# Kernel optimization log

Hardware: AMD Instinct MI355X
Metric: run time of the kernel (lower is better)

## Reference

```python
import jax, jax.numpy as jnp
import numpy as np

B, LQ, LK, D, H, DK, DV = 4, 2048, 2048, 1024, 16, 64, 64
TEMP = float(np.sqrt(DK))
LN_EPS = 1e-5


def setup_inputs() -> dict:
    key = jax.random.key(0)
    ks = jax.random.split(key, 12)
    std_qk = float(np.sqrt(2.0 / (D + DK)))
    std_v = float(np.sqrt(2.0 / (D + DV)))
    std_fc = float(np.sqrt(2.0 / (H * DV + D)))  # xavier normal
    return {
        "q": jax.random.normal(ks[0], (B, LQ, D), jnp.float32),
        "k": jax.random.normal(ks[1], (B, LK, D), jnp.float32),
        "v": jax.random.normal(ks[2], (B, LK, D), jnp.float32),
        "key_padding_mask": jax.random.randint(ks[3], (B, LK), 0, 2) > 0,
        "Wq": jax.random.normal(ks[4], (D, H * DK), jnp.float32) * std_qk,
        "bq": jnp.zeros((H * DK,), jnp.float32),
        "Wk": jax.random.normal(ks[5], (D, H * DK), jnp.float32) * std_qk,
        "bk": jnp.zeros((H * DK,), jnp.float32),
        "Wv": jax.random.normal(ks[6], (D, H * DV), jnp.float32) * std_v,
        "bv": jnp.zeros((H * DV,), jnp.float32),
        "Wo": jax.random.normal(ks[7], (H * DV, D), jnp.float32) * std_fc,
        "bo": jnp.zeros((D,), jnp.float32),
        "ln_g": jnp.ones((D,), jnp.float32),
        "ln_b": jnp.zeros((D,), jnp.float32),
    }


def reference(q, k, v, key_padding_mask, Wq, bq, Wk, bk, Wv, bv, Wo, bo, ln_g, ln_b):
    residual = q
    # projections -> [B, H, L, dh]
    qh = (q @ Wq + bq).reshape(B, LQ, H, DK).transpose(0, 2, 1, 3)
    kh = (k @ Wk + bk).reshape(B, LK, H, DK).transpose(0, 2, 1, 3)
    vh = (v @ Wv + bv).reshape(B, LK, H, DV).transpose(0, 2, 1, 3)
    # scaled dot-product attention, mask padded keys with -inf pre-softmax
    logits = jnp.einsum("bhqd,bhkd->bhqk", qh, kh) / TEMP
    logits = jnp.where(key_padding_mask[:, None, None, :], -jnp.inf, logits)
    attn = jax.nn.softmax(logits, axis=-1)  # masked entries -> 0
    out = jnp.einsum("bhqk,bhkd->bhqd", attn, vh)
    # concat heads (head-major per original permute) -> [B, LQ, H*DV]
    out = out.transpose(0, 2, 1, 3).reshape(B, LQ, H * DV)
    out = out @ Wo + bo
    out = out + residual  # skip connection (d_out == d_model)
    # LayerNorm over last dim
    mu = out.mean(-1, keepdims=True)
    var = ((out - mu) ** 2).mean(-1, keepdims=True)
    out = (out - mu) * jax.lax.rsqrt(var + LN_EPS) * ln_g + ln_b
    attn_avg = attn.mean(axis=1)  # average over heads -> [B, LQ, LK]
    return out, attn_avg
```

## Files before the change

kernel.cpp:

```cpp
#include <hip/hip_runtime.h>
#include <hip/hip_bf16.h>
#include <math.h>

#define B_    4
#define LQ_   2048
#define LK_   2048
#define D_    1024
#define H_    16
#define LN_EPS_ 1e-5f
#define NEGINF (-__builtin_inff())
#define QSCALE 0.18033688011112042f

typedef __attribute__((ext_vector_type(8))) short bf16x8;
typedef __attribute__((ext_vector_type(4))) short bf16x4;
typedef __attribute__((ext_vector_type(4))) float f32x4;

#define MFMA(a, b, c) __builtin_amdgcn_mfma_f32_16x16x32_bf16(a, b, c, 0, 0, 0)

#if __has_builtin(__builtin_amdgcn_exp2f)
#define EXP2(x) __builtin_amdgcn_exp2f(x)
#else
#define EXP2(x) __expf((x) * 0.6931471805599453f)
#endif

__device__ __forceinline__ short f2bf(float f) {
    union { __hip_bfloat16 h; short s; } u;
    u.h = __float2bfloat16(f);
    return u.s;
}

__device__ __forceinline__ void gld16(const short* g, short* l) {
    __builtin_amdgcn_global_load_lds(
        (const __attribute__((address_space(1))) void*)g,
        (__attribute__((address_space(3))) void*)l, 16, 0, 0);
}

__global__ __launch_bounds__(256) void zfill_kernel(float* __restrict__ p)
{
    const size_t i = ((size_t)blockIdx.x * 256 + threadIdx.x) * 4;
    *reinterpret_cast<f32x4*>(p + i) = (f32x4){0.f, 0.f, 0.f, 0.f};
}

__global__ __launch_bounds__(256) void scan_kernel(
    const int* __restrict__ mask, int* __restrict__ idx, int* __restrict__ pos,
    int* __restrict__ cnt, float* __restrict__ maskc)
{
    const int b = blockIdx.x;
    const int t = threadIdx.x;
    const int lane = t & 63, wid = t >> 6;
    __shared__ int wsum[4];
    const int base = b * 2048 + t * 8;

    int fl[8]; int loc = 0;
    #pragma unroll
    for (int j = 0; j < 8; ++j) { fl[j] = (mask[base + j] == 0) ? 1 : 0; loc += fl[j]; }

    int inc = loc;
    #pragma unroll
    for (int d = 1; d < 64; d <<= 1) {
        const int n = __shfl_up(inc, d);
        if (lane >= d) inc += n;
    }
    if (lane == 63) wsum[wid] = inc;
    __syncthreads();
    int wbase = 0;
    for (int i = 0; i < wid; ++i) wbase += wsum[i];
    const int total = wsum[0] + wsum[1] + wsum[2] + wsum[3];

    int e = wbase + inc - loc;
    #pragma unroll
    for (int j = 0; j < 8; ++j) {
        const int p = t * 8 + j;
        if (fl[j]) { idx[b * 2048 + e] = p; pos[base + j] = e; ++e; }
        else        pos[base + j] = -1;
        maskc[base + j] = (p < total) ? 0.f : NEGINF;
        if (p >= total) idx[base + j] = 0;
    }
    if (t == 0) cnt[b] = total;
}

__global__ __launch_bounds__(256) void cast_x_kernel(
    const float* __restrict__ q, const float* __restrict__ k, const float* __restrict__ v,
    short* __restrict__ Xq, short* __restrict__ Xk, short* __restrict__ Xv)
{
    const int which = blockIdx.y;
    const float* src = which == 0 ? q : (which == 1 ? k : v);
    short* dst       = which == 0 ? Xq : (which == 1 ? Xk : Xv);
    const int t = threadIdx.x;
    const size_t i = ((size_t)blockIdx.x * 256 + t) * 8;
    const float4 a = *reinterpret_cast<const float4*>(src + i);
    const float4 c = *reinterpret_cast<const float4*>(src + i + 4);
    bf16x8 o;
    o[0] = f2bf(a.x); o[1] = f2bf(a.y); o[2] = f2bf(a.z); o[3] = f2bf(a.w);
    o[4] = f2bf(c.x); o[5] = f2bf(c.y); o[6] = f2bf(c.z); o[7] = f2bf(c.w);
    *reinterpret_cast<bf16x8*>(dst + i) = o;
}

__global__ __launch_bounds__(256) void cast_wt_kernel(
    const float* __restrict__ Wq, const float* __restrict__ Wk,
    const float* __restrict__ Wv, const float* __restrict__ Wo,
    short* __restrict__ Wtq, short* __restrict__ Wtk,
    short* __restrict__ Wtv, short* __restrict__ Wto)
{
    const int which = blockIdx.z;
    const float* W = which == 0 ? Wq : (which == 1 ? Wk : (which == 2 ? Wv : Wo));
    short* Wt      = which == 0 ? Wtq : (which == 1 ? Wtk : (which == 2 ? Wtv : Wto));

    __shared__ float T[64][65];
    const int t = threadIdx.x;
    const int k0 = blockIdx.x * 64, n0 = blockIdx.y * 64;
    {
        const int row = t >> 2, cq = (t & 3) * 16;
        #pragma unroll
        for (int i = 0; i < 4; ++i) {
            const float4 v4 = *reinterpret_cast<const float4*>(&W[(size_t)(k0 + row) * 1024 + n0 + cq + i * 4]);
            T[row][cq + i * 4 + 0] = v4.x; T[row][cq + i * 4 + 1] = v4.y;
            T[row][cq + i * 4 + 2] = v4.z; T[row][cq + i * 4 + 3] = v4.w;
        }
    }
    __syncthreads();
    const int nl = t >> 2, kq = (t & 3) * 16;
    bf16x8 o0, o1;
    #pragma unroll
    for (int j = 0; j < 8; ++j) {
        o0[j] = f2bf(T[kq + j][nl]);
        o1[j] = f2bf(T[kq + 8 + j][nl]);
    }
    *reinterpret_cast<bf16x8*>(&Wt[(size_t)(n0 + nl) * 1024 + k0 + kq]) = o0;
    *reinterpret_cast<bf16x8*>(&Wt[(size_t)(n0 + nl) * 1024 + k0 + kq + 8]) = o1;
}

__global__ __launch_bounds__(256) void proj_kernel(
    const short* __restrict__ Xq, const short* __restrict__ Xk, const short* __restrict__ Xv,
    const short* __restrict__ Wtq, const short* __restrict__ Wtk, const short* __restrict__ Wtv,
    const float* __restrict__ bq, const float* __restrict__ bk, const float* __restrict__ bv,
    const int* __restrict__ pos,
    short* __restrict__ qh, short* __restrict__ kh, short* __restrict__ vTc)
{
    const int which = blockIdx.z;
    const short* A  = which == 0 ? Xq : (which == 1 ? Xk : Xv);
    const short* Bt = which == 0 ? Wtq : (which == 1 ? Wtk : Wtv);
    const float* bias = which == 0 ? bq : (which == 1 ? bk : bv);

    __shared__ short Al[4096];
    __shared__ short Bl[4096];

    const int t = threadIdx.x;
    const int lane = t & 63, w = t >> 6;
    const int wm = w >> 1, wn = w & 1;
    const int g = lane >> 4, r16 = lane & 15;
    const int m0 = blockIdx.y * 128, n0 = blockIdx.x * 128;

    f32x4 acc[4][4] = {};

    for (int k0 = 0; k0 < 1024; k0 += 32) {
        __syncthreads();
        #pragma unroll
        for (int i = 0; i < 2; ++i) {
            const int row = i * 64 + (t >> 2);
            const int cl = (t & 3) ^ ((row >> 1) & 3);
            gld16(A  + (size_t)(m0 + row) * 1024 + k0 + cl * 8, Al + i * 2048 + t * 8);
            gld16(Bt + (size_t)(n0 + row) * 1024 + k0 + cl * 8, Bl + i * 2048 + t * 8);
        }
        __syncthreads();

        bf16x8 af[4], bf[4];
        #pragma unroll
        for (int mf = 0; mf < 4; ++mf) {
            const int row = wm * 64 + mf * 16 + r16;
            af[mf] = *reinterpret_cast<const bf16x8*>(
                (const char*)Al + row * 64 + (((g ^ ((row >> 1) & 3))) << 4));
        }
        #pragma unroll
        for (int nf = 0; nf < 4; ++nf) {
            const int row = wn * 64 + nf * 16 + r16;
            bf[nf] = *reinterpret_cast<const bf16x8*>(
                (const char*)Bl + row * 64 + (((g ^ ((row >> 1) & 3))) << 4));
        }
        #pragma unroll
        for (int mf = 0; mf < 4; ++mf)
            #pragma unroll
            for (int nf = 0; nf < 4; ++nf)
                acc[mf][nf] = MFMA(af[mf], bf[nf], acc[mf][nf]);
    }

    if (which < 2) {
        #pragma unroll
        for (int nf = 0; nf < 4; ++nf) {
            const int n = n0 + wn * 64 + nf * 16 + r16;
            const int h = n >> 6, dh = n & 63;
            const float bn = bias[n];
            #pragma unroll
            for (int mf = 0; mf < 4; ++mf) {
                #pragma unroll
                for (int r = 0; r < 4; ++r) {
                    const int m = m0 + wm * 64 + mf * 16 + 4 * g + r;
                    const int bb = m >> 11, l = m & 2047;
                    float vf = acc[mf][nf][r] + bn;
                    if (which == 0) vf *= QSCALE;
                    ((which == 0) ? qh : kh)[(((size_t)(bb * H_ + h)) * LQ_ + l) * 64 + dh] = f2bf(vf);
                }
            }
        }
    } else {
        int posr[4][4], bbr[4][4];
        #pragma unroll
        for (int mf = 0; mf < 4; ++mf)
            #pragma unroll
            for (int r = 0; r < 4; ++r) {
                const int m = m0 + wm * 64 + mf * 16 + 4 * g + r;
                const int bb = m >> 11, l = m & 2047;
                bbr[mf][r] = bb;
                posr[mf][r] = pos[bb * 2048 + l];
            }
        #pragma unroll
        for (int nf = 0; nf < 4; ++nf) {
            const int n = n0 + wn * 64 + nf * 16 + r16;
            const int h = n >> 6, dh = n & 63;
            const float bn = bias[n];
            #pragma unroll
            for (int mf = 0; mf < 4; ++mf) {
                #pragma unroll
                for (int r = 0; r < 4; ++r) {
                    const int pc = posr[mf][r];
                    if (pc >= 0)
                        vTc[(((size_t)(bbr[mf][r] * H_ + h)) * 64 + dh) * (size_t)LK_ + pc] =
                            f2bf(acc[mf][nf][r] + bn);
                }
            }
        }
    }
}

__global__ __launch_bounds__(256) void flash_kernel(
    const short* __restrict__ qh, const short* __restrict__ kh, const short* __restrict__ vTc,
    const int* __restrict__ idx, const int* __restrict__ cnt, const float* __restrict__ maskc,
    short* __restrict__ ctx, float* __restrict__ mOut, float* __restrict__ sOut)
{
    const int q0 = blockIdx.x * 64;
    const int h  = blockIdx.y;
    const int b  = blockIdx.z;

    __shared__ short Kl[2][4096];
    __shared__ short Vl[2][4096];

    const int t = threadIdx.x;
    const int lane = t & 63, w = t >> 6;
    const int g = lane >> 4, q16 = lane & 15;

    const short* kbase = kh + (size_t)(b * H_ + h) * LK_ * 64;
    const short* vbase = vTc + (size_t)(b * H_ + h) * 64 * (size_t)LK_;
    const int*   idxb  = idx + b * 2048;
    const int nt = (cnt[b] + 63) >> 6;

    bf16x8 qf0, qf1;
    {
        const short* qrow = qh + ((size_t)(b * H_ + h) * LQ_ + q0 + w * 16 + q16) * 64;
        qf0 = *reinterpret_cast<const bf16x8*>(qrow + 8 * g);
        qf1 = *reinterpret_cast<const bf16x8*>(qrow + 32 + 8 * g);
    }

    f32x4 mlast[4] = {};
    if (nt > 0) {
        #pragma unroll
        for (int kb = 0; kb < 4; ++kb)
            mlast[kb] = *reinterpret_cast<const f32x4*>(
                maskc + b * 2048 + (nt - 1) * 64 + kb * 16 + 4 * g);
    }

    const int srw = t >> 3, scl = t & 7;

    f32x4 ot[4] = {};
    float m_run = NEGINF, l_run = 0.f;

    if (nt > 0) {
        #pragma unroll
        for (int i = 0; i < 2; ++i) {
            const int row = i * 32 + srw;
            const int cl = scl ^ (row & 7);
            const int orig = idxb[row];
            gld16(kbase + (size_t)orig * 64 + cl * 8, Kl[0] + i * 2048 + t * 8);
            gld16(vbase + (size_t)row * LK_ + cl * 8, Vl[0] + i * 2048 + t * 8);
        }
    }
    __syncthreads();

    int cur = 0;
    for (int kt = 0; kt < nt; ++kt) {
        if (kt + 1 < nt) {
            const int kn = (kt + 1) * 64;
            #pragma unroll
            for (int i = 0; i < 2; ++i) {
                const int row = i * 32 + srw;
                const int cl = scl ^ (row & 7);
                const int orig = idxb[kn + row];
                gld16(kbase + (size_t)orig * 64 + cl * 8, Kl[cur ^ 1] + i * 2048 + t * 8);
                gld16(vbase + (size_t)row * LK_ + kn + cl * 8, Vl[cur ^ 1] + i * 2048 + t * 8);
            }
        }
        const bool lastt = (kt == nt - 1);

        float lg[4][4];
        const short* klp = Kl[cur];
        __builtin_amdgcn_s_setprio(1);
        #pragma unroll
        for (int kb = 0; kb < 4; ++kb) {
            const int krow = kb * 16 + q16;
            const char* rowp = (const char*)klp + krow * 128;
            const int sw = (krow & 7) << 4;
            const bf16x8 kf0 = *reinterpret_cast<const bf16x8*>(rowp + ((g << 4) ^ sw));
            const bf16x8 kf1 = *reinterpret_cast<const bf16x8*>(rowp + (((4 + g) << 4) ^ sw));
            f32x4 s = lastt ? mlast[kb] : (f32x4){0.f, 0.f, 0.f, 0.f};
            s = MFMA(kf0, qf0, s);
            s = MFMA(kf1, qf1, s);
            #pragma unroll
            for (int r = 0; r < 4; ++r) lg[kb][r] = s[r];
        }
        __builtin_amdgcn_s_setprio(0);

        float tm = NEGINF;
        #pragma unroll
        for (int kb = 0; kb < 4; ++kb)
            #pragma unroll
            for (int r = 0; r < 4; ++r) tm = fmaxf(tm, lg[kb][r]);
        tm = fmaxf(tm, __shfl_xor(tm, 16));
        tm = fmaxf(tm, __shfl_xor(tm, 32));

        const bool skip = __all(tm <= m_run + 8.0f);
        if (!skip) {
            const float m_new = fmaxf(m_run, tm);
            const float alpha = (m_run == NEGINF) ? 0.f : EXP2(m_run - m_new);
            #pragma unroll
            for (int fc = 0; fc < 4; ++fc)
                #pragma unroll
                for (int r = 0; r < 4; ++r) ot[fc][r] *= alpha;
            l_run *= alpha;
            m_run = m_new;
        }
        const float m_use = (m_run == NEGINF) ? 0.f : m_run;

        float p[4][4];
        float ls = 0.f;
        #pragma unroll
        for (int kb = 0; kb < 4; ++kb)
            #pragma unroll
            for (int r = 0; r < 4; ++r) { p[kb][r] = EXP2(lg[kb][r] - m_use); ls += p[kb][r]; }
        ls += __shfl_xor(ls, 16);
        ls += __shfl_xor(ls, 32);
        l_run += ls;

        bf16x8 pb[2];
        #pragma unroll
        for (int r = 0; r < 4; ++r) {
            pb[0][r]     = f2bf(p[0][r]);
            pb[0][4 + r] = f2bf(p[1][r]);
            pb[1][r]     = f2bf(p[2][r]);
            pb[1][4 + r] = f2bf(p[3][r]);
        }

        const short* vlp = Vl[cur];
        __builtin_amdgcn_s_setprio(1);
        #pragma unroll
        for (int fc = 0; fc < 4; ++fc) {
            const int dvrow = fc * 16 + q16;
            const char* rowp = (const char*)vlp + dvrow * 128;
            const int sw = (dvrow & 7) << 4;
            #pragma unroll
            for (int tt = 0; tt < 2; ++tt) {
                const bf16x4 va = *reinterpret_cast<const bf16x4*>(rowp + ((64 * tt + 8 * g) ^ sw));
                const bf16x4 vb = *reinterpret_cast<const bf16x4*>(rowp + ((64 * tt + 32 + 8 * g) ^ sw));
                bf16x8 af;
                af[0] = va[0]; af[1] = va[1]; af[2] = va[2]; af[3] = va[3];
                af[4] = vb[0]; af[5] = vb[1]; af[6] = vb[2]; af[7] = vb[3];
                ot[fc] = MFMA(af, pb[tt], ot[fc]);
            }
        }
        __builtin_amdgcn_s_setprio(0);

        __syncthreads();
        cur ^= 1;
    }

    const float rs = (l_run > 0.f) ? 1.0f / l_run : 0.f;
    short* crow = ctx + ((size_t)b * LQ_ + q0 + w * 16 + q16) * (size_t)(H_ * 64) + h * 64;
    #pragma unroll
    for (int fc = 0; fc < 4; ++fc) {
        bf16x4 o4;
        #pragma unroll
        for (int r = 0; r < 4; ++r) o4[r] = f2bf(ot[fc][r] * rs);
        *reinterpret_cast<bf16x4*>(crow + fc * 16 + 4 * g) = o4;
    }
    if (lane < 16) {
        const size_t idxo = (size_t)(b * H_ + h) * LQ_ + q0 + w * 16 + lane;
        mOut[idxo] = m_run;
        sOut[idxo] = l_run;
    }
}

__global__ __launch_bounds__(256) void avg_kernel(
    const short* __restrict__ qh, const short* __restrict__ kh,
    const int* __restrict__ idx, const int* __restrict__ cnt,
    const float* __restrict__ maskc,
    const float* __restrict__ mS, const float* __restrict__ sS,
    float* __restrict__ attn_avg)
{
    const int b = blockIdx.z;
    const int cntb = cnt[b];
    const int nt = (cntb + 63) >> 6;
    if ((int)blockIdx.x >= nt) return;

    const int kc0 = blockIdx.x * 64;
    const int q0  = blockIdx.y * 64;

    __shared__ short Kl[2][4096];

    const int t = threadIdx.x;
    const int lane = t & 63, w = t >> 6;
    const int g = lane >> 4, q16 = lane & 15;

    f32x4 mk[4];
    #pragma unroll
    for (int kb = 0; kb < 4; ++kb)
        mk[kb] = *reinterpret_cast<const f32x4*>(maskc + b * 2048 + kc0 + kb * 16 + 4 * g);

    const int srw = t >> 3, scl = t & 7;
    const size_t khbase = (size_t)b * H_ * (size_t)LK_ * 64;
    const int* idxb = idx + b * 2048;

    const int orig0 = idxb[kc0 + srw];
    const int orig1 = idxb[kc0 + 32 + srw];
    const int cl = scl ^ (srw & 7);

    const short* qbase = qh + ((size_t)b * H_ * LQ_ + q0 + w * 16 + q16) * 64;
    const size_t stbase = (size_t)b * H_ * LQ_ + q0 + w * 16 + q16;

    {
        gld16(kh + khbase + (size_t)orig0 * 64 + cl * 8, Kl[0] + t * 8);
        gld16(kh + khbase + (size_t)orig1 * 64 + cl * 8, Kl[0] + 2048 + t * 8);
    }
    bf16x8 qf0 = *reinterpret_cast<const bf16x8*>(qbase + 8 * g);
    bf16x8 qf1 = *reinterpret_cast<const bf16x8*>(qbase + 32 + 8 * g);
    float mrow = mS[stbase], srv = sS[stbase];
    __syncthreads();

    f32x4 acc[4] = {};
    int cur = 0;
    for (int hh = 0; hh < H_; ++hh) {
        bf16x8 qn0, qn1; float mn = 0.f, sn = 0.f;
        if (hh + 1 < H_) {
            const size_t hb = khbase + (size_t)(hh + 1) * LK_ * 64;
            gld16(kh + hb + (size_t)orig0 * 64 + cl * 8, Kl[cur ^ 1] + t * 8);
            gld16(kh + hb + (size_t)orig1 * 64 + cl * 8, Kl[cur ^ 1] + 2048 + t * 8);
            const short* qb2 = qbase + (size_t)(hh + 1) * LQ_ * 64;
            qn0 = *reinterpret_cast<const bf16x8*>(qb2 + 8 * g);
            qn1 = *reinterpret_cast<const bf16x8*>(qb2 + 32 + 8 * g);
            mn = mS[stbase + (size_t)(hh + 1) * LQ_];
            sn = sS[stbase + (size_t)(hh + 1) * LQ_];
        }

        const float madj = (mrow == NEGINF || srv <= 0.f)
                               ? __builtin_inff() : mrow + __log2f(srv);

        const short* klp = Kl[cur];
        __builtin_amdgcn_s_setprio(1);
        #pragma unroll
        for (int kb = 0; kb < 4; ++kb) {
            const int krow = kb * 16 + q16;
            const char* rowp = (const char*)klp + krow * 128;
            const int sw = (krow & 7) << 4;
            const bf16x8 kf0 = *reinterpret_cast<const bf16x8*>(rowp + ((g << 4) ^ sw));
            const bf16x8 kf1 = *reinterpret_cast<const bf16x8*>(rowp + (((4 + g) << 4) ^ sw));
            f32x4 s = mk[kb];
            s = MFMA(kf0, qf0, s);
            s = MFMA(kf1, qf1, s);
            #pragma unroll
            for (int r = 0; r < 4; ++r)
                acc[kb][r] += EXP2(s[r] - madj);
        }
        __builtin_amdgcn_s_setprio(0);

        __syncthreads();
        if (hh + 1 < H_) { qf0 = qn0; qf1 = qn1; mrow = mn; srv = sn; }
        cur ^= 1;
    }

    const float sc = 1.0f / (float)H_;
    float* orow = attn_avg + ((size_t)b * LQ_ + q0 + w * 16 + q16) * (size_t)LK_;
    #pragma unroll
    for (int kb = 0; kb < 4; ++kb) {
        #pragma unroll
        for (int r = 0; r < 4; ++r) {
            const int kc = kc0 + kb * 16 + 4 * g + r;
            if (kc < cntb) orow[idxb[kc]] = acc[kb][r] * sc;
        }
    }
}

__global__ __launch_bounds__(256) void outproj_kernel(
    const short* __restrict__ ctxIn, const short* __restrict__ Wto,
    const float* __restrict__ bo, const float* __restrict__ resid,
    float* __restrict__ preln)
{
    __shared__ short Al[4096];
    __shared__ short Bl[4096];

    const int t = threadIdx.x;
    const int lane = t & 63, w = t >> 6;
    const int wm = w >> 1, wn = w & 1;
    const int g = lane >> 4, r16 = lane & 15;
    const int m0 = blockIdx.y * 128, n0 = blockIdx.x * 128;

    f32x4 acc[4][4] = {};

    for (int k0 = 0; k0 < 1024; k0 += 32) {
        __syncthreads();
        #pragma unroll
        for (int i = 0; i < 2; ++i) {
            const int row = i * 64 + (t >> 2);
            const int cl = (t & 3) ^ ((row >> 1) & 3);
            gld16(ctxIn + (size_t)(m0 + row) * 1024 + k0 + cl * 8, Al + i * 2048 + t * 8);
            gld16(Wto   + (size_t)(n0 + row) * 1024 + k0 + cl * 8, Bl + i * 2048 + t * 8);
        }
        __syncthreads();

        bf16x8 af[4], bf[4];
        #pragma unroll
        for (int mf = 0; mf < 4; ++mf) {
            const int row = wm * 64 + mf * 16 + r16;
            af[mf] = *reinterpret_cast<const bf16x8*>(
                (const char*)Al + row * 64 + (((g ^ ((row >> 1) & 3))) << 4));
        }
        #pragma unroll
        for (int nf = 0; nf < 4; ++nf) {
            const int row = wn * 64 + nf * 16 + r16;
            bf[nf] = *reinterpret_cast<const bf16x8*>(
                (const char*)Bl + row * 64 + (((g ^ ((row >> 1) & 3))) << 4));
        }
        #pragma unroll
        for (int mf = 0; mf < 4; ++mf)
            #pragma unroll
            for (int nf = 0; nf < 4; ++nf)
                acc[mf][nf] = MFMA(af[mf], bf[nf], acc[mf][nf]);
    }

    #pragma unroll
    for (int nf = 0; nf < 4; ++nf) {
        const int n = n0 + wn * 64 + nf * 16 + r16;
        const float bn = bo[n];
        #pragma unroll
        for (int mf = 0; mf < 4; ++mf) {
            #pragma unroll
            for (int r = 0; r < 4; ++r) {
                const size_t m = m0 + wm * 64 + mf * 16 + 4 * g + r;
                preln[m * 1024 + n] = acc[mf][nf][r] + bn + resid[m * 1024 + n];
            }
        }
    }
}

__global__ __launch_bounds__(256) void ln_kernel(
    const float* __restrict__ xin, const float* __restrict__ gam,
    const float* __restrict__ bet, float* __restrict__ out)
{
    const size_t row = blockIdx.x;
    const int t = threadIdx.x;
    const float4 v = *reinterpret_cast<const float4*>(&xin[row * 1024 + t * 4]);

    float s  = v.x + v.y + v.z + v.w;
    float ss = v.x * v.x + v.y * v.y + v.z * v.z + v.w * v.w;
    #pragma unroll
    for (int w = 1; w < 64; w <<= 1) { s += __shfl_xor(s, w); ss += __shfl_xor(ss, w); }

    __shared__ float rs_[4], rss_[4];
    if ((t & 63) == 0) { rs_[t >> 6] = s; rss_[t >> 6] = ss; }
    __syncthreads();
    s  = rs_[0] + rs_[1] + rs_[2] + rs_[3];
    ss = rss_[0] + rss_[1] + rss_[2] + rss_[3];

    const float mean = s * (1.0f / 1024.0f);
    const float var  = ss * (1.0f / 1024.0f) - mean * mean;
    const float rstd = rsqrtf(var + LN_EPS_);

    const float4 g4 = *reinterpret_cast<const float4*>(&gam[t * 4]);
    const float4 b4 = *reinterpret_cast<const float4*>(&bet[t * 4]);
    float4 o;
    o.x = (v.x - mean) * rstd * g4.x + b4.x;
    o.y = (v.y - mean) * rstd * g4.y + b4.y;
    o.z = (v.z - mean) * rstd * g4.z + b4.z;
    o.w = (v.w - mean) * rstd * g4.w + b4.w;
    *reinterpret_cast<float4*>(&out[row * 1024 + t * 4]) = o;
}

extern "C" void kernel_launch(void* const* d_in, const int* in_sizes, int n_in,
                              void* d_out, int out_size, void* d_ws, size_t ws_size,
                              hipStream_t stream)
{
    const float* q    = (const float*)d_in[0];
    const float* k    = (const float*)d_in[1];
    const float* v    = (const float*)d_in[2];
    const int*   mask = (const int*)d_in[3];
    const float* Wq   = (const float*)d_in[4];
    const float* bq   = (const float*)d_in[5];
    const float* Wk   = (const float*)d_in[6];
    const float* bk   = (const float*)d_in[7];
    const float* Wv   = (const float*)d_in[8];
    const float* bv   = (const float*)d_in[9];
    const float* Wo   = (const float*)d_in[10];
    const float* bo   = (const float*)d_in[11];
    const float* lng  = (const float*)d_in[12];
    const float* lnb  = (const float*)d_in[13];

    float* out      = (float*)d_out;
    float* attn_avg = out + (size_t)B_ * LQ_ * D_;

    const size_t XSZ = (size_t)B_ * LQ_ * D_;
    const size_t WSZ = (size_t)D_ * D_;

    short* Xq  = (short*)d_ws;
    short* Xk  = Xq + XSZ;
    short* Xv  = Xk + XSZ;
    short* Wtq = Xv + XSZ;
    short* Wtk = Wtq + WSZ;
    short* Wtv = Wtk + WSZ;
    short* Wto = Wtv + WSZ;
    short* qh  = Wto + WSZ;
    short* kh  = qh + XSZ;
    short* vTc = kh + XSZ;
    float* mSt = (float*)(vTc + XSZ);
    float* sSt = mSt + (size_t)B_ * H_ * LQ_;
    float* maskc = sSt + (size_t)B_ * H_ * LQ_;
    int*   idx   = (int*)(maskc + (size_t)B_ * LK_);
    int*   pos   = idx + (size_t)B_ * LK_;
    int*   cnt   = pos + (size_t)B_ * LK_;
    float* preln = (float*)qh;
    short* ctx   = Xv;

    zfill_kernel<<<dim3((B_ * LQ_ * LK_) / (256 * 4)), 256, 0, stream>>>(attn_avg);
    scan_kernel<<<dim3(B_), 256, 0, stream>>>(mask, idx, pos, cnt, maskc);
    cast_x_kernel<<<dim3(4096, 3), 256, 0, stream>>>(q, k, v, Xq, Xk, Xv);
    cast_wt_kernel<<<dim3(16, 16, 4), 256, 0, stream>>>(Wq, Wk, Wv, Wo, Wtq, Wtk, Wtv, Wto);

    proj_kernel<<<dim3(8, 64, 3), 256, 0, stream>>>(Xq, Xk, Xv, Wtq, Wtk, Wtv,
                                                    bq, bk, bv, pos, qh, kh, vTc);

    flash_kernel<<<dim3(32, 16, 4), 256, 0, stream>>>(qh, kh, vTc, idx, cnt, maskc,
                                                      ctx, mSt, sSt);

    avg_kernel<<<dim3(32, 32, 4), 256, 0, stream>>>(qh, kh, idx, cnt, maskc,
                                                    mSt, sSt, attn_avg);

    outproj_kernel<<<dim3(8, 64), 256, 0, stream>>>(ctx, Wto, bo, q, preln);

    ln_kernel<<<8192, 256, 0, stream>>>(preln, lng, lnb, out);
}
```

Before: 367.9 us.

## Deepen avg_kernel K prefetch to a five-buffer ring with manual vmcnt waits

```diff
diff --git a/kernel.cpp b/kernel.cpp
--- a/kernel.cpp
+++ b/kernel.cpp
@@ -412,7 +412,7 @@
     const int kc0 = blockIdx.x * 64;
     const int q0  = blockIdx.y * 64;
 
-    __shared__ short Kl[2][4096];
+    __shared__ short Kl[5][4096];
 
     const int t = threadIdx.x;
     const int lane = t & 63, w = t >> 6;
@@ -424,44 +424,54 @@
         mk[kb] = *reinterpret_cast<const f32x4*>(maskc + b * 2048 + kc0 + kb * 16 + 4 * g);
 
     const int srw = t >> 3, scl = t & 7;
-    const size_t khbase = (size_t)b * H_ * (size_t)LK_ * 64;
     const int* idxb = idx + b * 2048;
-
     const int orig0 = idxb[kc0 + srw];
     const int orig1 = idxb[kc0 + 32 + srw];
     const int cl = scl ^ (srw & 7);
 
+    const short* kp0 = kh + (size_t)b * H_ * (size_t)LK_ * 64 + (size_t)orig0 * 64 + cl * 8;
+    const short* kp1 = kh + (size_t)b * H_ * (size_t)LK_ * 64 + (size_t)orig1 * 64 + cl * 8;
+    const size_t hstep = (size_t)LK_ * 64;
+
     const short* qbase = qh + ((size_t)b * H_ * LQ_ + q0 + w * 16 + q16) * 64;
     const size_t stbase = (size_t)b * H_ * LQ_ + q0 + w * 16 + q16;
 
-    {
-        gld16(kh + khbase + (size_t)orig0 * 64 + cl * 8, Kl[0] + t * 8);
-        gld16(kh + khbase + (size_t)orig1 * 64 + cl * 8, Kl[0] + 2048 + t * 8);
-    }
-    bf16x8 qf0 = *reinterpret_cast<const bf16x8*>(qbase + 8 * g);
-    bf16x8 qf1 = *reinterpret_cast<const bf16x8*>(qbase + 32 + 8 * g);
-    float mrow = mS[stbase], srv = sS[stbase];
-    __syncthreads();
+    #define KSTAGE_(hh, bi) { \
+        gld16(kp0 + (size_t)(hh) * hstep, Kl[bi] + t * 8); \
+        gld16(kp1 + (size_t)(hh) * hstep, Kl[bi] + 2048 + t * 8); }
+    #define QLOAD_(hh, qa, qb, mm, ss) { \
+        const short* qp_ = qbase + (size_t)(hh) * LQ_ * 64; \
+        qa = *reinterpret_cast<const bf16x8*>(qp_ + 8 * g); \
+        qb = *reinterpret_cast<const bf16x8*>(qp_ + 32 + 8 * g); \
+        mm = mS[stbase + (size_t)(hh) * LQ_]; \
+        ss = sS[stbase + (size_t)(hh) * LQ_]; }
+
+    bf16x8 qc0, qc1, qn0, qn1, ql0, ql1;
+    float mc, sc, mn, sn, ml, sl;
+
+    KSTAGE_(0, 0);
+    QLOAD_(0, qc0, qc1, mc, sc);
+    KSTAGE_(1, 1);
+    QLOAD_(1, qn0, qn1, mn, sn);
+    KSTAGE_(2, 2);
 
     f32x4 acc[4] = {};
-    int cur = 0;
+    int bget = 0, bput = 3;
+
     for (int hh = 0; hh < H_; ++hh) {
-        bf16x8 qn0, qn1; float mn = 0.f, sn = 0.f;
-        if (hh + 1 < H_) {
-            const size_t hb = khbase + (size_t)(hh + 1) * LK_ * 64;
-            gld16(kh + hb + (size_t)orig0 * 64 + cl * 8, Kl[cur ^ 1] + t * 8);
-            gld16(kh + hb + (size_t)orig1 * 64 + cl * 8, Kl[cur ^ 1] + 2048 + t * 8);
-            const short* qb2 = qbase + (size_t)(hh + 1) * LQ_ * 64;
-            qn0 = *reinterpret_cast<const bf16x8*>(qb2 + 8 * g);
-            qn1 = *reinterpret_cast<const bf16x8*>(qb2 + 32 + 8 * g);
-            mn = mS[stbase + (size_t)(hh + 1) * LQ_];
-            sn = sS[stbase + (size_t)(hh + 1) * LQ_];
-        }
-
-        const float madj = (mrow == NEGINF || srv <= 0.f)
-                               ? __builtin_inff() : mrow + __log2f(srv);
-
-        const short* klp = Kl[cur];
+        const int hq = (hh + 2 < H_) ? hh + 2 : H_ - 1;
+        QLOAD_(hq, ql0, ql1, ml, sl);
+        const int hk = (hh + 3 < H_) ? hh + 3 : H_ - 1;
+        KSTAGE_(hk, bput);
+
+        asm volatile("s_waitcnt vmcnt(12)" ::: "memory");
+        __builtin_amdgcn_s_barrier();
+        asm volatile("" ::: "memory");
+
+        const float madj = (mc == NEGINF || sc <= 0.f)
+                               ? __builtin_inff() : mc + __log2f(sc);
+
+        const short* klp = Kl[bget];
         __builtin_amdgcn_s_setprio(1);
         #pragma unroll
         for (int kb = 0; kb < 4; ++kb) {
@@ -471,29 +481,35 @@
             const bf16x8 kf0 = *reinterpret_cast<const bf16x8*>(rowp + ((g << 4) ^ sw));
             const bf16x8 kf1 = *reinterpret_cast<const bf16x8*>(rowp + (((4 + g) << 4) ^ sw));
             f32x4 s = mk[kb];
-            s = MFMA(kf0, qf0, s);
-            s = MFMA(kf1, qf1, s);
+            s = MFMA(kf0, qc0, s);
+            s = MFMA(kf1, qc1, s);
             #pragma unroll
             for (int r = 0; r < 4; ++r)
                 acc[kb][r] += EXP2(s[r] - madj);
         }
         __builtin_amdgcn_s_setprio(0);
 
-        __syncthreads();
-        if (hh + 1 < H_) { qf0 = qn0; qf1 = qn1; mrow = mn; srv = sn; }
-        cur ^= 1;
-    }
-
-    const float sc = 1.0f / (float)H_;
+        qc0 = qn0; qc1 = qn1; mc = mn; sc = sn;
+        qn0 = ql0; qn1 = ql1; mn = ml; sn = sl;
+        bget = (bget == 4) ? 0 : bget + 1;
+        bput = (bput == 4) ? 0 : bput + 1;
+    }
+
+    asm volatile("s_waitcnt vmcnt(0)" ::: "memory");
+    __builtin_amdgcn_s_barrier();
+
+    const float scale = 1.0f / (float)H_;
     float* orow = attn_avg + ((size_t)b * LQ_ + q0 + w * 16 + q16) * (size_t)LK_;
     #pragma unroll
     for (int kb = 0; kb < 4; ++kb) {
         #pragma unroll
         for (int r = 0; r < 4; ++r) {
             const int kc = kc0 + kb * 16 + 4 * g + r;
-            if (kc < cntb) orow[idxb[kc]] = acc[kb][r] * sc;
-        }
-    }
+            if (kc < cntb) orow[idxb[kc]] = acc[kb][r] * scale;
+        }
+    }
+    #undef KSTAGE_
+    #undef QLOAD_
 }
 
 __global__ __launch_bounds__(256) void outproj_kernel(
```

Result: slower. 382.9 us (+4.1%).
